# Optimization experiments

Measured on AMD Instinct MI355X. Metric: run time of the kernel, lower is better.

## Reference

```python
import jax, jax.numpy as jnp
import numpy as np

FILL = -1000.0


def setup_inputs() -> dict:
    key = jax.random.key(0)
    k1, k2, k3 = jax.random.split(key, 3)
    B, T, L = 512, 512, 126
    emissions = jax.random.normal(k1, (B, T, L), dtype=jnp.float32)
    labels = jax.random.randint(k2, (B, T), 0, L, dtype=jnp.int32)
    transitions = jax.random.normal(k3, (L + 2, L + 2), dtype=jnp.float32)
    # mask: nothing transitions INTO start; nothing transitions OUT of end
    transitions = transitions.at[:, L].set(FILL).at[L + 1, :].set(FILL)
    return {"emissions": emissions, "labels": labels, "transitions": transitions}


def _expand_emission(emission, L):
    # emission: [T, L] -> [T+2, L+2] with START/END pseudo-observations
    T = emission.shape[0]
    pad = jnp.full((T, 2), FILL, dtype=emission.dtype)
    e = jnp.concatenate([emission, pad], axis=1)
    b_s = jnp.full((1, L + 2), FILL, dtype=emission.dtype).at[0, L].set(0.0)
    e_s = jnp.full((1, L + 2), FILL, dtype=emission.dtype).at[0, L + 1].set(0.0)
    return jnp.concatenate([b_s, e, e_s], axis=0)


def _total_path_score(emission, transitions, L):
    # Faithful to the original _log_sum_exp: per-column max, but the log term
    # sums exp over the WHOLE matrix (scalar), added to every column max.
    E = _expand_emission(emission, L)  # [T+2, L+2]

    def step(pre, obs):
        score = obs[None, :] + pre[:, None] + transitions  # [L+2, L+2]
        m = jnp.max(score, axis=0)                         # [L+2]
        pre_new = m + jnp.log(jnp.sum(jnp.exp(score - m[None, :])))
        return pre_new, None

    pre, _ = jax.lax.scan(step, E[0], E[1:])
    m = jnp.max(pre)
    return m + jnp.log(jnp.sum(jnp.exp(pre - m)))


def _real_path_score(emission, labels, transitions, L):
    T = emission.shape[0]
    em = jnp.sum(emission[jnp.arange(T), labels])
    seq = jnp.concatenate([
        jnp.array([L], dtype=labels.dtype), labels,
        jnp.array([L + 1], dtype=labels.dtype)
    ])
    tr = jnp.sum(transitions[seq[:-1], seq[1:]])
    return em + tr


def reference(emissions, labels, transitions):
    L = emissions.shape[-1]
    total = jax.vmap(lambda e: _total_path_score(e, transitions, L))(emissions)
    real = jax.vmap(lambda e, y: _real_path_score(e, y, transitions, L))(emissions, labels)
    return jnp.sum(total - real)
```

## Files before the change

kernel.cpp:

```cpp
#include <hip/hip_runtime.h>
#include <hip/hip_fp16.h>

#define NB 512
#define NT 512
#define NL 126
#define NS 128
#define SIGMA 0.0625f

typedef _Float16 h2 __attribute__((ext_vector_type(2)));

static __device__ __forceinline__ int pk_from(float a, float b) {
  return __builtin_bit_cast(int, __builtin_amdgcn_cvt_pkrtz(a, b));
}
static __device__ __forceinline__ int pkmul(int a, int b) {
  int d; asm("v_pk_mul_f16 %0, %1, %2" : "=v"(d) : "v"(a), "v"(b)); return d;
}
static __device__ __forceinline__ int pkmax(int a, int b) {
  int d; asm("v_pk_max_f16 %0, %1, %2" : "=v"(d) : "v"(a), "v"(b)); return d;
}
static __device__ __forceinline__ int pkadd(int a, int b) {
  int d; asm("v_pk_add_f16 %0, %1, %2" : "=v"(d) : "v"(a), "v"(b)); return d;
}

#define WAVE_ADD(x) do { \
  asm("v_add_f32_dpp %0, %0, %0 row_shr:1  row_mask:0xf bank_mask:0xf bound_ctrl:0" : "+v"(x)); \
  asm("v_add_f32_dpp %0, %0, %0 row_shr:2  row_mask:0xf bank_mask:0xf bound_ctrl:0" : "+v"(x)); \
  asm("v_add_f32_dpp %0, %0, %0 row_shr:4  row_mask:0xf bank_mask:0xf bound_ctrl:0" : "+v"(x)); \
  asm("v_add_f32_dpp %0, %0, %0 row_shr:8  row_mask:0xf bank_mask:0xf bound_ctrl:0" : "+v"(x)); \
  asm("v_add_f32_dpp %0, %0, %0 row_bcast:15 row_mask:0xa bank_mask:0xf bound_ctrl:0" : "+v"(x)); \
  asm("v_add_f32_dpp %0, %0, %0 row_bcast:31 row_mask:0xc bank_mask:0xf bound_ctrl:0" : "+v"(x)); \
} while (0)

__global__ __launch_bounds__(128) __attribute__((amdgpu_waves_per_eu(1, 1)))
void crf_kernel(
    const float* __restrict__ emissions,
    const int*   __restrict__ labels,
    const float* __restrict__ trans,
    float*       __restrict__ out)
{
  const int b   = blockIdx.x;
  const int tid = threadIdx.x;
  const int wv  = tid >> 6;
  const int ln  = tid & 63;
  const int col = tid;
  const bool has = (col < NL);

  __shared__ __align__(16) _Float16 u_sh[2][NS];
  __shared__ float sPart[2][2];
  __shared__ float zPart[2][2];
  __shared__ float fin[2];

  const float* em  = emissions + (size_t)b * NT * NL;
  const int*   lab = labels + (size_t)b * NT;

  float tau = -3.0e38f;
  for (int rr = 0; rr < NS; rr++) tau = fmaxf(tau, trans[rr * NS + col]);

  int tab[64];
  #pragma unroll
  for (int k = 0; k < 64; k++) {
    float t0 = __expf(trans[(2 * k) * NS + col] - tau);
    float t1 = __expf(trans[(2 * k + 1) * NS + col] - tau);
    tab[k] = pk_from(t0, t1);
  }

  float realp = 0.f;
  #pragma unroll
  for (int q = 0; q < NT / 128; q++) {
    int t  = tid + q * 128;
    int la = lab[t];
    int na = (t + 1 < NT) ? lab[t + 1] : (NL + 1);
    realp += em[t * NL + la] + trans[la * NS + na];
  }
  if (tid == 0) realp += trans[NL * NS + lab[0]];

  u_sh[0][col] = (_Float16)((col == NL) ? 1.f : 0.f);

  float emc = has ? em[col] : 0.f;
  float emn = has ? em[NL + col] : 0.f;

  float Cc = 0.f, Q = 0.f;
  __syncthreads();

  #pragma unroll 2
  for (int t = 0; t <= NT; t++) {
    const int sl = t & 1;

    float r;
    if (t > 0) {
      float S = sPart[sl][0] + sPart[sl][1];
      float Z = zPart[sl][0] + zPart[sl][1];
      Cc += __logf(S);
      Q  += __logf(Z);
      r = SIGMA * __builtin_amdgcn_rcpf(Z);
    } else {
      r = SIGMA;
    }

    float obs;
    if (t < NT) obs = has ? emc : -1000.f;
    else        obs = (col == NL + 1) ? 0.f : -1000.f;
    float g = __expf(obs + tau);

    float ef = (t + 2 < NT && has) ? em[(t + 2) * NL + col] : 0.f;
    emc = emn; emn = ef;

    const int4* up = (const int4*)u_sh[sl];
    int4 uu[16];
    #pragma unroll
    for (int j = 0; j < 16; j++) uu[j] = up[j];

    int ha = 0, hb = 0, hcc = 0, hd = 0;
    int sa = 0, sb = 0, scc = 0, sd = 0;
    #pragma unroll
    for (int j = 0; j < 16; j++) {
      int m;
      m = pkmul(uu[j].x, tab[4*j+0]); ha  = pkmax(ha,  m); sa  = pkadd(sa,  m);
      m = pkmul(uu[j].y, tab[4*j+1]); hb  = pkmax(hb,  m); sb  = pkadd(sb,  m);
      m = pkmul(uu[j].z, tab[4*j+2]); hcc = pkmax(hcc, m); scc = pkadd(scc, m);
      m = pkmul(uu[j].w, tab[4*j+3]); hd  = pkmax(hd,  m); sd  = pkadd(sd,  m);
    }
    int hv = pkmax(pkmax(ha, hb), pkmax(hcc, hd));
    int sv = pkadd(pkadd(sa, sb), pkadd(scc, sd));
    h2 hh = __builtin_bit_cast(h2, hv);
    h2 ss = __builtin_bit_cast(h2, sv);
    float h = fmaxf(fmaxf((float)hh.x, (float)hh.y), 1e-30f);
    float s = (float)ss.x + (float)ss.y;

    float w = h * g;
    float v = w * r;
    u_sh[sl ^ 1][col] = (_Float16)v;

    float contrib = s * __builtin_amdgcn_rcpf(h);
    float zz = v;
    WAVE_ADD(contrib);
    WAVE_ADD(zz);
    if (ln == 63) {
      sPart[sl ^ 1][wv] = contrib;
      zPart[sl ^ 1][wv] = zz;
    }
    __syncthreads();
  }

  {
    float S = sPart[1][0] + sPart[1][1];
    float Z = zPart[1][0] + zPart[1][1];
    Cc += __logf(S);
    Q  += __logf(Z);
  }

  WAVE_ADD(realp);
  if (ln == 63) fin[wv] = realp;
  __syncthreads();
  if (tid == 0) {
    const float CONST = 513.f * 2.772588722f;
    atomicAdd(out, (Cc + Q + CONST) - (fin[0] + fin[1]));
  }
}

extern "C" void kernel_launch(void* const* d_in, const int* in_sizes, int n_in,
                              void* d_out, int out_size, void* d_ws, size_t ws_size,
                              hipStream_t stream) {
  const float* em  = (const float*)d_in[0];
  const int*   lab = (const int*)d_in[1];
  const float* tr  = (const float*)d_in[2];
  (void)hipMemsetAsync(d_out, 0, sizeof(float), stream);
  crf_kernel<<<NB, 128, 0, stream>>>(em, lab, tr, (float*)d_out);
}
```

Before: 577.5 us.

## Defer column-sum reduction off the critical path and use lighter barrier

Moves the per-column s/h contribution reduction out of the serial recurrence. It is computed at the end of one step and reduced and logged during the next step, with a dummy initial value that contributes log(1)=0. The full __syncthreads is replaced by an LDS waitcnt plus a raw s_barrier, and the emission prefetch uses a running pointer instead of recomputing the index. The aim is to shorten the latency chain between barriers, at the cost of more delicate ordering of the shared-memory double buffer.

Result: no change. 586.1 us (+1.5%).

```diff
diff --git a/kernel.cpp b/kernel.cpp
--- a/kernel.cpp
+++ b/kernel.cpp
@@ -31,6 +31,12 @@
   asm("v_add_f32_dpp %0, %0, %0 row_bcast:31 row_mask:0xc bank_mask:0xf bound_ctrl:0" : "+v"(x)); \
 } while (0)
 
+#define LIGHT_BARRIER() do { \
+  asm volatile("s_waitcnt lgkmcnt(0)" ::: "memory"); \
+  __builtin_amdgcn_s_barrier(); \
+  asm volatile("" ::: "memory"); \
+} while (0)
+
 __global__ __launch_bounds__(128) __attribute__((amdgpu_waves_per_eu(1, 1)))
 void crf_kernel(
     const float* __restrict__ emissions,
@@ -46,7 +52,7 @@
   const bool has = (col < NL);
 
   __shared__ __align__(16) _Float16 u_sh[2][NS];
-  __shared__ float sPart[2][2];
+  __shared__ float sPartC[2][2];
   __shared__ float zPart[2][2];
   __shared__ float fin[2];
 
@@ -75,9 +81,12 @@
   if (tid == 0) realp += trans[NL * NS + lab[0]];
 
   u_sh[0][col] = (_Float16)((col == NL) ? 1.f : 0.f);
+  if (tid < 2) sPartC[1][tid] = 0.5f;
+  float cS = 1.f / 128.f;
 
   float emc = has ? em[col] : 0.f;
   float emn = has ? em[NL + col] : 0.f;
+  const float* emp = em + 2 * NL + col;
 
   float Cc = 0.f, Q = 0.f;
   __syncthreads();
@@ -86,12 +95,14 @@
   for (int t = 0; t <= NT; t++) {
     const int sl = t & 1;
 
+    WAVE_ADD(cS);
+    if (ln == 63) sPartC[sl][wv] = cS;
+    Cc += __logf(sPartC[sl ^ 1][0] + sPartC[sl ^ 1][1]);
+
     float r;
     if (t > 0) {
-      float S = sPart[sl][0] + sPart[sl][1];
       float Z = zPart[sl][0] + zPart[sl][1];
-      Cc += __logf(S);
-      Q  += __logf(Z);
+      Q += __logf(Z);
       r = SIGMA * __builtin_amdgcn_rcpf(Z);
     } else {
       r = SIGMA;
@@ -102,7 +113,9 @@
     else        obs = (col == NL + 1) ? 0.f : -1000.f;
     float g = __expf(obs + tau);
 
-    float ef = (t + 2 < NT && has) ? em[(t + 2) * NL + col] : 0.f;
+    float ef = 0.f;
+    if (t + 2 < NT && has) ef = *emp;
+    emp += NL;
     emc = emn; emn = ef;
 
     const int4* up = (const int4*)u_sh[sl];
@@ -131,22 +144,23 @@
     float v = w * r;
     u_sh[sl ^ 1][col] = (_Float16)v;
 
-    float contrib = s * __builtin_amdgcn_rcpf(h);
     float zz = v;
-    WAVE_ADD(contrib);
     WAVE_ADD(zz);
-    if (ln == 63) {
-      sPart[sl ^ 1][wv] = contrib;
-      zPart[sl ^ 1][wv] = zz;
-    }
-    __syncthreads();
+    if (ln == 63) zPart[sl ^ 1][wv] = zz;
+
+    cS = s * __builtin_amdgcn_rcpf(h);
+
+    LIGHT_BARRIER();
   }
 
+  WAVE_ADD(cS);
+  if (ln == 63) sPartC[1][wv] = cS;
+  __syncthreads();
+  Cc += __logf(sPartC[0][0] + sPartC[0][1]);
+  Cc += __logf(sPartC[1][0] + sPartC[1][1]);
   {
-    float S = sPart[1][0] + sPart[1][1];
     float Z = zPart[1][0] + zPart[1][1];
-    Cc += __logf(S);
-    Q  += __logf(Z);
+    Q += __logf(Z);
   }
 
   WAVE_ADD(realp);
```
